# Kernel tuning notes

Measured on AMD Instinct MI355X. Metric: run time of the kernel, lower is better.

The kernel has to match this reference:

```python
import jax, jax.numpy as jnp
import numpy as np

EPS = 1e-12  # F.normalize default eps

def _unfold3(x):
    # torch F.unfold(kernel=(3,3), padding=1): [B,C,H,W] -> [B, C*9, H*W]
    # channel-major, kernel offsets row-major (matches torch ordering)
    B, C, H, W = x.shape
    xp = jnp.pad(x, ((0, 0), (0, 0), (1, 1), (1, 1)))
    p = jnp.stack([xp[:, :, i:i + H, j:j + W] for i in range(3) for j in range(3)], axis=2)  # [B,C,9,H,W]
    return p.reshape(B, C * 9, H * W)

def _fold3(u, H, W):
    # torch F.fold(output_size=(H,W), kernel=(3,3), padding=1): sums overlapping patches
    B, CK, L = u.shape
    C = CK // 9
    p = u.reshape(B, C, 3, 3, H, W)
    out = jnp.zeros((B, C, H + 2, W + 2), u.dtype)
    for i in range(3):
        for j in range(3):
            out = out.at[:, :, i:i + H, j:j + W].add(p[:, :, i, j])
    return out[:, :, 1:H + 1, 1:W + 1]

def setup_inputs() -> dict:
    key = jax.random.key(0)
    k1, k2, k3 = jax.random.split(key, 3)
    B, C, H, W = 4, 64, 64, 64
    return {
        "lrsr_lv3": jax.random.normal(k1, (B, C, H, W), jnp.float32),
        "refsr_lv3": jax.random.normal(k2, (B, C, H, W), jnp.float32),
        "ref_lv3": jax.random.normal(k3, (B, C, H, W), jnp.float32),
    }

def reference(lrsr_lv3, refsr_lv3, ref_lv3):
    B, C, H, W = lrsr_lv3.shape
    lr_u = _unfold3(lrsr_lv3)                         # [B, D, L_lr], D = C*9
    rs_u = _unfold3(refsr_lv3).transpose(0, 2, 1)     # [B, L_ref, D]
    rs_u = rs_u / jnp.maximum(jnp.linalg.norm(rs_u, axis=2, keepdims=True), EPS)
    lr_u = lr_u / jnp.maximum(jnp.linalg.norm(lr_u, axis=1, keepdims=True), EPS)
    corr = jnp.einsum('brd,bdl->brl', rs_u, lr_u)     # [B, L_ref, L_lr]
    s = jnp.max(corr, axis=1)                         # [B, L_lr]
    arg = jnp.argmax(corr, axis=1)                    # [B, L_lr]
    ref_u = _unfold3(ref_lv3)                         # [B, D, L_ref]
    trans_u = jnp.take_along_axis(ref_u, arg[:, None, :], axis=2)  # [B, D, L_lr]
    trans_lv3 = _fold3(trans_u, H, W)                 # [B, C, H, W]
    return s.reshape(B, 1, H, W), trans_lv3
```

## Files before the change

kernel.cpp:

```cpp
#include <hip/hip_runtime.h>

#define BATCH 4
#define CH    64
#define HH    64
#define WW    64
#define LL    4096
#define SPLITS 4
#define RPS   1024
#define NRT   4

#define RSTB  112
#define BUFB  57344
#define BSOFF 28672
#define CSTRIDE 139392

#define PAD_L   4356
#define GP_BYTE_BASE 1048576
#define GP_SIDE_STRIDE 6690816
#define GP_B_STRIDE    1672704
#define GP_COMP_STRIDE 557568
#define GP_TOTAL       13381632

#define WS_SSQ_RS 0
#define WS_SSQ_LR 16384
#define WS_INV_RS 32768
#define WS_INV_LR 49152
#define WS_PMAX   65536
#define WS_PARG   131072
#define WS_ARG    196608

typedef __attribute__((ext_vector_type(8))) short short8b;
typedef __attribute__((ext_vector_type(4))) float f32x4;
typedef __attribute__((ext_vector_type(16))) float f32x16;

__device__ __forceinline__ void gload16(const void* g, void* l) {
    __builtin_amdgcn_global_load_lds(
        (const __attribute__((address_space(1))) unsigned int*)g,
        (__attribute__((address_space(3))) unsigned int*)l, 16, 0, 0);
}

__global__ void k_split(const float* __restrict__ lrsr,
                        const float* __restrict__ refsr,
                        float* __restrict__ ws) {
    int tid  = threadIdx.x;
    int pos  = blockIdx.x * 256 + tid;
    int c8   = blockIdx.y;
    int side = blockIdx.z >> 2;
    int b    = blockIdx.z & 3;
    const float* src = (side ? lrsr : refsr) + (size_t)b * CH * LL + c8 * 8 * LL + pos;
    int ppos = (pos >> 6) * 66 + (pos & 63) + 67;
    char* dst = (char*)ws + GP_BYTE_BASE + side * GP_SIDE_STRIDE + b * GP_B_STRIDE
              + (size_t)(c8 * PAD_L + ppos) * 16;
    union { unsigned short u[8]; uint4 v; } w0, w1, w2;
    #pragma unroll
    for (int cc = 0; cc < 8; ++cc) {
        float x = src[cc * LL];
        unsigned u0 = __float_as_uint(x);
        float f0 = __uint_as_float(u0 & 0xffff0000u);
        float r1 = x - f0;
        unsigned u1 = __float_as_uint(r1);
        float f1 = __uint_as_float(u1 & 0xffff0000u);
        float r2 = r1 - f1;
        w0.u[cc] = (unsigned short)(u0 >> 16);
        w1.u[cc] = (unsigned short)(u1 >> 16);
        w2.u[cc] = (unsigned short)(__float_as_uint(r2) >> 16);
    }
    *(uint4*)(dst)                      = w0.v;
    *(uint4*)(dst + GP_COMP_STRIDE)     = w1.v;
    *(uint4*)(dst + 2 * GP_COMP_STRIDE) = w2.v;
}

__global__ void k_ssq(const float* __restrict__ lrsr,
                      const float* __restrict__ refsr,
                      float* __restrict__ ws) {
    int t = blockIdx.x * 256 + threadIdx.x;
    int b = t >> 12;
    int r = t & (LL - 1);
    const float* pl = lrsr + (size_t)b * CH * LL + r;
    const float* pr = refsr + (size_t)b * CH * LL + r;
    float sl = 0.f, sr = 0.f;
    #pragma unroll 8
    for (int c = 0; c < CH; ++c) {
        float a = pl[c * LL]; sl += a * a;
        float d = pr[c * LL]; sr += d * d;
    }
    ws[WS_SSQ_RS + t] = sr;
    ws[WS_SSQ_LR + t] = sl;
}

__global__ void k_inv(float* __restrict__ ws) {
    int t = blockIdx.x * 256 + threadIdx.x;
    int b = t >> 12;
    int r = t & (LL - 1);
    int y = r >> 6, x = r & 63;
    float srs = 0.f, slr = 0.f;
    for (int di = -1; di <= 1; ++di) {
        int yy = y + di;
        if ((unsigned)yy >= (unsigned)HH) continue;
        for (int dj = -1; dj <= 1; ++dj) {
            int xx = x + dj;
            if ((unsigned)xx >= (unsigned)WW) continue;
            int idx = b * LL + yy * WW + xx;
            srs += ws[WS_SSQ_RS + idx];
            slr += ws[WS_SSQ_LR + idx];
        }
    }
    ws[WS_INV_RS + t] = 1.f / fmaxf(sqrtf(srs), 1e-12f);
    ws[WS_INV_LR + t] = 1.f / fmaxf(sqrtf(slr), 1e-12f);
}

__global__ __launch_bounds__(512, 2)
void k_corrmax(float* __restrict__ ws) {
    __shared__ __align__(16) char LDSB[2 * BUFB];

    int tid  = threadIdx.x;
    int L    = blockIdx.x;
    int xcd  = L & 7;
    int slot = L >> 3;
    int b    = xcd >> 1;
    int bx   = slot >> 1;
    int by   = ((xcd & 1) << 1) | (slot & 1);
    int l0   = bx * 256;
    int rbs  = by * RPS;

    int lane = tid & 63;
    int w    = __builtin_amdgcn_readfirstlane(tid >> 6);
    int wr   = w >> 2;
    int wc   = w & 3;
    int l31  = lane & 31;
    int g2   = lane >> 5;

    const float* invn_rs = ws + WS_INV_RS + b * LL;
    const char*  gpB = (const char*)ws + GP_BYTE_BASE + b * GP_B_STRIDE;

    int LC[7];
    int sideF[7];
    #pragma unroll
    for (int n = 0; n < 7; ++n) {
        int G    = n * 512 + tid;
        int side = (n * 8 + w >= 28) ? 1 : 0;
        int gg   = G - side * 1792;
        int row  = gg / 7;
        int slot2 = gg - row * 7;
        int comp = (slot2 >= 6) ? 0 : (slot2 >> 1);
        int oct  = (slot2 >= 6) ? 0 : (slot2 & 1);
        LC[n] = side * GP_SIDE_STRIDE + comp * GP_COMP_STRIDE + oct * (PAD_L * 16)
              + (row + 2 * (row >> 6)) * 16;
        sideF[n] = side;
    }

    int abase = (wr * 128 + l31) * RSTB + g2 * 16;
    int bbase = BSOFF + (wc * 64 + l31) * RSTB + g2 * 16;

    int ybA = by * 16;
    int ybB = bx * 4;

    auto issue = [&](int rt2, int q2, int m2, int bufo) {
        int i2 = (q2 < 3) ? -1 : ((q2 < 6) ? 0 : 1);
        int j2 = q2 - (i2 + 1) * 3 - 1;
        int suA = ((ybA + rt2 * 4 + 1 + i2) * 66 + 1 + j2) * 16 + m2 * CSTRIDE;
        int suB = ((ybB + 1 + i2) * 66 + 1 + j2) * 16 + m2 * CSTRIDE;
        #pragma unroll
        for (int n = 0; n < 7; ++n) {
            int su = sideF[n] ? suB : suA;
            gload16(gpB + (LC[n] + su), LDSB + bufo + n * 8192 + tid * 16);
        }
    };

    float rm[2] = {-1e30f, -1e30f};
    int   ra[2] = {0, 0};

    issue(0, 0, 0, 0);
    int cur = 0;

    for (int rt = 0; rt < NRT; ++rt) {
        int r0 = rbs + rt * 256;

        f32x16 acc[4][2];
        #pragma unroll
        for (int mf = 0; mf < 4; ++mf)
            #pragma unroll
            for (int nf = 0; nf < 2; ++nf)
                #pragma unroll
                for (int e = 0; e < 16; ++e) acc[mf][nf][e] = 0.f;

        for (int q = 0; q < 9; ++q) {
            for (int m = 0; m < 4; ++m) {
                __syncthreads();
                {
                    int m2 = m + 1, q2 = q, rt2 = rt;
                    if (m2 == 4) { m2 = 0; ++q2; if (q2 == 9) { q2 = 0; ++rt2; } }
                    if (rt2 < NRT) issue(rt2, q2, m2, (cur ^ 1) * BUFB);
                }
                const char* lb = LDSB + cur * BUFB;
                short8b bfr[2][3];
                #pragma unroll
                for (int nf = 0; nf < 2; ++nf)
                    #pragma unroll
                    for (int c = 0; c < 3; ++c)
                        bfr[nf][c] = *(const short8b*)(lb + bbase + nf * (32 * RSTB) + c * 32);
                #pragma unroll
                for (int mfh = 0; mfh < 2; ++mfh) {
                    short8b afr[2][3];
                    #pragma unroll
                    for (int mi = 0; mi < 2; ++mi)
                        #pragma unroll
                        for (int c = 0; c < 3; ++c)
                            afr[mi][c] = *(const short8b*)(lb + abase + (mfh * 2 + mi) * (32 * RSTB) + c * 32);
                    __builtin_amdgcn_s_setprio(1);
                    #pragma unroll
                    for (int mi = 0; mi < 2; ++mi)
                        #pragma unroll
                        for (int nf = 0; nf < 2; ++nf) {
                            f32x16 d = acc[mfh * 2 + mi][nf];
                            d = __builtin_amdgcn_mfma_f32_32x32x16_bf16(afr[mi][0], bfr[nf][0], d, 0, 0, 0);
                            d = __builtin_amdgcn_mfma_f32_32x32x16_bf16(afr[mi][0], bfr[nf][1], d, 0, 0, 0);
                            d = __builtin_amdgcn_mfma_f32_32x32x16_bf16(afr[mi][1], bfr[nf][0], d, 0, 0, 0);
                            d = __builtin_amdgcn_mfma_f32_32x32x16_bf16(afr[mi][1], bfr[nf][1], d, 0, 0, 0);
                            d = __builtin_amdgcn_mfma_f32_32x32x16_bf16(afr[mi][0], bfr[nf][2], d, 0, 0, 0);
                            d = __builtin_amdgcn_mfma_f32_32x32x16_bf16(afr[mi][2], bfr[nf][0], d, 0, 0, 0);
                            acc[mfh * 2 + mi][nf] = d;
                        }
                    __builtin_amdgcn_s_setprio(0);
                }
                cur ^= 1;
            }
        }

        #pragma unroll
        for (int mf = 0; mf < 4; ++mf) {
            f32x4 iv[4];
            #pragma unroll
            for (int rb = 0; rb < 4; ++rb)
                iv[rb] = *(const f32x4*)&invn_rs[r0 + wr * 128 + mf * 32 + g2 * 4 + rb * 8];
            #pragma unroll
            for (int nf = 0; nf < 2; ++nf)
                #pragma unroll
                for (int reg = 0; reg < 16; ++reg) {
                    int r = r0 + wr * 128 + mf * 32 + (reg & 3) + 8 * (reg >> 2) + 4 * g2;
                    float val = acc[mf][nf][reg] * iv[reg >> 2][reg & 3];
                    if (val > rm[nf] || (val == rm[nf] && r < ra[nf])) { rm[nf] = val; ra[nf] = r; }
                }
        }
    }

    #pragma unroll
    for (int nf = 0; nf < 2; ++nf) {
        float ov = __shfl_xor(rm[nf], 32);
        int   oi = __shfl_xor(ra[nf], 32);
        if (ov > rm[nf] || (ov == rm[nf] && oi < ra[nf])) { rm[nf] = ov; ra[nf] = oi; }
    }
    __syncthreads();
    float* sm2 = (float*)LDSB;
    int*   si2 = (int*)LDSB + 512;
    if (lane < 32) {
        #pragma unroll
        for (int nf = 0; nf < 2; ++nf) {
            sm2[wr * 256 + wc * 64 + nf * 32 + l31] = rm[nf];
            si2[wr * 256 + wc * 64 + nf * 32 + l31] = ra[nf];
        }
    }
    __syncthreads();
    if (tid < 256) {
        float bm = sm2[tid]; int ba = si2[tid];
        float v  = sm2[256 + tid]; int a2 = si2[256 + tid];
        if (v > bm || (v == bm && a2 < ba)) { bm = v; ba = a2; }
        int l = l0 + tid;
        int o = (b * SPLITS + by) * LL + l;
        ws[WS_PMAX + o] = bm;
        ((int*)ws)[WS_PARG + o] = ba;
    }
}

__global__ void k_reduce(float* __restrict__ ws, float* __restrict__ out) {
    int t = blockIdx.x * 256 + threadIdx.x;
    int b = t >> 12;
    int l = t & (LL - 1);
    float bm = -1e30f; int ba = 0;
    for (int s = 0; s < SPLITS; ++s) {
        int o = (b * SPLITS + s) * LL + l;
        float v = ws[WS_PMAX + o];
        int   a = ((int*)ws)[WS_PARG + o];
        if (v > bm || (v == bm && a < ba)) { bm = v; ba = a; }
    }
    out[t] = bm * ws[WS_INV_LR + t];
    ((int*)ws)[WS_ARG + t] = ba;
}

__global__ void k_fold(const float* __restrict__ ref,
                       const float* __restrict__ ws,
                       float* __restrict__ out) {
    int t = blockIdx.x * 256 + threadIdx.x;
    int b = t >> 18;
    int c = (t >> 12) & 63;
    int yx = t & (LL - 1);
    int y = yx >> 6, x = yx & 63;
    const int* ab = ((const int*)ws) + WS_ARG + b * LL;
    const float* rb = ref + (size_t)b * CH * LL + c * LL;
    float s = 0.f;
    #pragma unroll
    for (int i = 0; i < 3; ++i) {
        int yp = y + 1 - i;
        if ((unsigned)yp >= (unsigned)HH) continue;
        #pragma unroll
        for (int j = 0; j < 3; ++j) {
            int xp = x + 1 - j;
            if ((unsigned)xp >= (unsigned)WW) continue;
            int r = ab[yp * WW + xp];
            int ry = (r >> 6) + i - 1;
            int rx = (r & 63) + j - 1;
            if ((unsigned)ry < (unsigned)HH && (unsigned)rx < (unsigned)WW)
                s += rb[ry * WW + rx];
        }
    }
    out[BATCH * LL + t] = s;
}

extern "C" void kernel_launch(void* const* d_in, const int* in_sizes, int n_in,
                              void* d_out, int out_size, void* d_ws, size_t ws_size,
                              hipStream_t stream) {
    const float* lrsr = (const float*)d_in[0];
    const float* refsr = (const float*)d_in[1];
    const float* ref  = (const float*)d_in[2];
    float* out = (float*)d_out;
    float* ws  = (float*)d_ws;

    hipMemsetAsync((char*)d_ws + GP_BYTE_BASE, 0, GP_TOTAL, stream);
    k_split<<<dim3(16, 8, 8), dim3(256), 0, stream>>>(lrsr, refsr, ws);
    k_ssq<<<dim3(BATCH * LL / 256), dim3(256), 0, stream>>>(lrsr, refsr, ws);
    k_inv<<<dim3(BATCH * LL / 256), dim3(256), 0, stream>>>(ws);
    k_corrmax<<<dim3(256), dim3(512), 0, stream>>>(ws);
    k_reduce<<<dim3(BATCH * LL / 256), dim3(256), 0, stream>>>(ws, out);
    k_fold<<<dim3(BATCH * CH * LL / 256), dim3(256), 0, stream>>>(ref, ws, out);
}
```

Before: 400.9 us.

## Triple-buffer LDS staging with vmcnt waits and slot-major tile layout

Replaces the double-buffered LDS pipeline with three buffers, so loads are issued two stages ahead. Each stage waits on vmcnt for only the oldest load group before a raw s_barrier, instead of a full __syncthreads. The LDS tile layout also moves from padded row-stride records to slot-major 8KB planes, with 6 loads per thread instead of 7, dropping the unused padding slot. The goal is more latency hiding for global-to-LDS transfers and simpler addressing. The cost is more LDS per block (144KB), which may limit occupancy against the launch bound of 2 blocks, and fragment reads may hit new bank conflicts.

```diff
diff --git a/kernel.cpp b/kernel.cpp
--- a/kernel.cpp
+++ b/kernel.cpp
@@ -9,9 +9,9 @@
 #define RPS   1024
 #define NRT   4
 
-#define RSTB  112
-#define BUFB  57344
-#define BSOFF 28672
+#define BUFB  49152
+#define BSOFF 24576
+#define NBUF3 147456
 #define CSTRIDE 139392
 
 #define PAD_L   4356
@@ -111,15 +111,15 @@
 
 __global__ __launch_bounds__(512, 2)
 void k_corrmax(float* __restrict__ ws) {
-    __shared__ __align__(16) char LDSB[2 * BUFB];
+    __shared__ __align__(16) char LDSB[NBUF3];
 
     int tid  = threadIdx.x;
     int L    = blockIdx.x;
     int xcd  = L & 7;
-    int slot = L >> 3;
+    int slt  = L >> 3;
     int b    = xcd >> 1;
-    int bx   = slot >> 1;
-    int by   = ((xcd & 1) << 1) | (slot & 1);
+    int bx   = slt >> 1;
+    int by   = ((xcd & 1) << 1) | (slt & 1);
     int l0   = bx * 256;
     int rbs  = by * RPS;
 
@@ -133,24 +133,19 @@
     const float* invn_rs = ws + WS_INV_RS + b * LL;
     const char*  gpB = (const char*)ws + GP_BYTE_BASE + b * GP_B_STRIDE;
 
-    int LC[7];
-    int sideF[7];
+    int LC[6];
     #pragma unroll
-    for (int n = 0; n < 7; ++n) {
-        int G    = n * 512 + tid;
-        int side = (n * 8 + w >= 28) ? 1 : 0;
-        int gg   = G - side * 1792;
-        int row  = gg / 7;
-        int slot2 = gg - row * 7;
-        int comp = (slot2 >= 6) ? 0 : (slot2 >> 1);
-        int oct  = (slot2 >= 6) ? 0 : (slot2 & 1);
-        LC[n] = side * GP_SIDE_STRIDE + comp * GP_COMP_STRIDE + oct * (PAD_L * 16)
-              + (row + 2 * (row >> 6)) * 16;
-        sideF[n] = side;
-    }
-
-    int abase = (wr * 128 + l31) * RSTB + g2 * 16;
-    int bbase = BSOFF + (wc * 64 + l31) * RSTB + g2 * 16;
+    for (int n = 0; n < 6; ++n) {
+        int side = (n >= 3) ? 1 : 0;
+        int gg   = n * 512 + tid - side * 1536;
+        int slot = gg >> 8;
+        int pos  = gg & 255;
+        LC[n] = side * GP_SIDE_STRIDE + (slot >> 1) * GP_COMP_STRIDE
+              + (slot & 1) * (PAD_L * 16) + (pos + 2 * (pos >> 6)) * 16;
+    }
+
+    int abase = g2 * 4096 + (wr * 128 + l31) * 16;
+    int bbase = BSOFF + g2 * 4096 + (wc * 64 + l31) * 16;
 
     int ybA = by * 16;
     int ybB = bx * 4;
@@ -161,8 +156,8 @@
         int suA = ((ybA + rt2 * 4 + 1 + i2) * 66 + 1 + j2) * 16 + m2 * CSTRIDE;
         int suB = ((ybB + 1 + i2) * 66 + 1 + j2) * 16 + m2 * CSTRIDE;
         #pragma unroll
-        for (int n = 0; n < 7; ++n) {
-            int su = sideF[n] ? suB : suA;
+        for (int n = 0; n < 6; ++n) {
+            int su = (n >= 3) ? suB : suA;
             gload16(gpB + (LC[n] + su), LDSB + bufo + n * 8192 + tid * 16);
         }
     };
@@ -171,7 +166,10 @@
     int   ra[2] = {0, 0};
 
     issue(0, 0, 0, 0);
-    int cur = 0;
+    issue(0, 0, 1, BUFB);
+    int ibrt = 0, ibq = 0, ibm = 2;
+    int bufn = 2 * BUFB;
+    int bufc = 0;
 
     for (int rt = 0; rt < NRT; ++rt) {
         int r0 = rbs + rt * 256;
@@ -186,19 +184,26 @@
 
         for (int q = 0; q < 9; ++q) {
             for (int m = 0; m < 4; ++m) {
-                __syncthreads();
-                {
-                    int m2 = m + 1, q2 = q, rt2 = rt;
-                    if (m2 == 4) { m2 = 0; ++q2; if (q2 == 9) { q2 = 0; ++rt2; } }
-                    if (rt2 < NRT) issue(rt2, q2, m2, (cur ^ 1) * BUFB);
+                if (rt == NRT - 1 && q == 8 && m == 3)
+                    asm volatile("s_waitcnt vmcnt(0)" ::: "memory");
+                else
+                    asm volatile("s_waitcnt vmcnt(6)" ::: "memory");
+                __builtin_amdgcn_s_barrier();
+
+                if (ibrt < NRT) {
+                    issue(ibrt, ibq, ibm, bufn);
+                    ++ibm;
+                    if (ibm == 4) { ibm = 0; ++ibq; if (ibq == 9) { ibq = 0; ++ibrt; } }
+                    bufn += BUFB; if (bufn == NBUF3) bufn = 0;
                 }
-                const char* lb = LDSB + cur * BUFB;
+
+                const char* lb = LDSB + bufc;
                 short8b bfr[2][3];
                 #pragma unroll
                 for (int nf = 0; nf < 2; ++nf)
                     #pragma unroll
                     for (int c = 0; c < 3; ++c)
-                        bfr[nf][c] = *(const short8b*)(lb + bbase + nf * (32 * RSTB) + c * 32);
+                        bfr[nf][c] = *(const short8b*)(lb + bbase + c * 8192 + nf * 512);
                 #pragma unroll
                 for (int mfh = 0; mfh < 2; ++mfh) {
                     short8b afr[2][3];
@@ -206,7 +211,7 @@
                     for (int mi = 0; mi < 2; ++mi)
                         #pragma unroll
                         for (int c = 0; c < 3; ++c)
-                            afr[mi][c] = *(const short8b*)(lb + abase + (mfh * 2 + mi) * (32 * RSTB) + c * 32);
+                            afr[mi][c] = *(const short8b*)(lb + abase + c * 8192 + (mfh * 2 + mi) * 512);
                     __builtin_amdgcn_s_setprio(1);
                     #pragma unroll
                     for (int mi = 0; mi < 2; ++mi)
@@ -223,7 +228,7 @@
                         }
                     __builtin_amdgcn_s_setprio(0);
                 }
-                cur ^= 1;
+                bufc += BUFB; if (bufc == NBUF3) bufc = 0;
             }
         }
 
```

New measurement: 376.2 us. 1.07x faster.
